# Kernel tuning notes

Hardware: AMD Instinct MI355X
Metric: run time of the kernel (lower is better)

Reference implementation:

```python
import jax, jax.numpy as jnp
import numpy as np

B, R, D, G = 1024, 256, 512, 4
BETA_GROUP = 6.0
BETA_K = 8.0
INIT_KAPPA = 6.0


def setup_inputs() -> dict:
    key = jax.random.key(0)
    ks = jax.random.split(key, 9)
    f32 = jnp.float32
    return {
        "x": jax.random.normal(ks[0], (B, D), f32),
        "th": 0.1 * jax.random.normal(ks[1], (R, D), f32),
        "ineq_sign_param": 0.1 * jax.random.normal(ks[2], (R, D), f32),
        "e_sign_param": 0.1 * jax.random.normal(ks[3], (R, D), f32),
        "mask_logit": jnp.full((R, D), -2.0, f32) + 0.01 * jax.random.normal(ks[4], (R, D), f32),
        "log_kappa": jnp.asarray(np.log(INIT_KAPPA), f32),
        "group_logits": 0.1 * jax.random.normal(ks[5], (G, D), f32),
        "tg": 0.1 * jax.random.normal(ks[6], (R, G), f32),
        "gmask_logit": jnp.full((R, G), -1.0, f32) + 0.01 * jax.random.normal(ks[7], (R, G), f32),
        "k_frac_param": jnp.zeros((R,), f32),
        "head_w": 0.01 * jax.random.normal(ks[8], (1, R), f32),
        "head_b": jnp.zeros((1,), f32),
    }


def reference(x, th, ineq_sign_param, e_sign_param, mask_logit, log_kappa,
              group_logits, tg, gmask_logit, k_frac_param, head_w, head_b):
    kappa = jnp.clip(jnp.exp(log_kappa), 0.5, 50.0)
    ineq = jnp.tanh(ineq_sign_param)                       # (R, D)
    # c: (B, R, D) sharp per-feature comparison
    c = jax.nn.sigmoid(kappa * ineq[None] * (x[:, None, :] - th[None]))
    m = jax.nn.sigmoid(mask_logit)                         # (R, D)
    e_sign = jnp.tanh(e_sign_param)                        # (R, D)
    sym = (m * e_sign)[None] * (2.0 * c - 1.0)             # (B, R, D)
    A = jax.nn.softmax(group_logits, axis=0)               # (G, D)
    eg = jnp.einsum('brd,gd->brg', sym, A)                 # (B, R, G)
    pg = jax.nn.sigmoid(BETA_GROUP * (eg - tg[None]))
    gmask = jax.nn.sigmoid(gmask_logit)                    # (R, G)
    score = jnp.sum(pg * gmask[None], axis=2)              # (B, R)
    enabled = jnp.sum(gmask, axis=1)[None] + 1e-6          # (1, R)
    k = jax.nn.sigmoid(k_frac_param)[None] * enabled       # (1, R)
    z = jax.nn.sigmoid(BETA_K * (score - k))               # (B, R)
    y = z @ head_w.T + head_b                              # (B, 1)
    return y.squeeze(-1)
```

## Files before the change

### kernel.cpp

```cpp
#include <hip/hip_runtime.h>

#define B 1024
#define R 256
#define D 512
#define G 4

#define LOG2E 1.44269504088896340736f

#define OFF_FA   0
#define OFF_FB   (R*D)
#define OFF_SAG  (2*R*D)
#define OFF_EPI  (2*R*D + G*R*D)
#define OFF_PART (OFF_EPI + R*12)
#define NRG 32
#define NBG 16

__device__ __forceinline__ float sig_precise(float v) {
    return 1.0f / (1.0f + expf(-v));
}

__global__ __launch_bounds__(256)
void sge_precompute(const float* __restrict__ th,  const float* __restrict__ isp,
                    const float* __restrict__ esp, const float* __restrict__ ml,
                    const float* __restrict__ lk,  const float* __restrict__ gl,
                    const float* __restrict__ tg,  const float* __restrict__ gml,
                    const float* __restrict__ kf,  const float* __restrict__ hw,
                    float* __restrict__ ws)
{
    const int r   = blockIdx.x;
    const int tid = threadIdx.x;
    __shared__ float4 red[256];

    float kappa = expf(lk[0]);
    kappa = fminf(fmaxf(kappa, 0.5f), 50.0f);

    float4 psum = make_float4(0.f, 0.f, 0.f, 0.f);
    for (int d = tid; d < D; d += 256) {
        const int idx = r * D + d;
        const float thv  = th[idx];
        const float ineq = tanhf(isp[idx]);
        const float es   = tanhf(esp[idx]);
        const float mm   = sig_precise(ml[idx]);
        const float g0 = gl[0*D + d], g1 = gl[1*D + d], g2 = gl[2*D + d], g3 = gl[3*D + d];
        const float mx = fmaxf(fmaxf(g0, g1), fmaxf(g2, g3));
        const float e0 = expf(g0 - mx), e1 = expf(g1 - mx), e2 = expf(g2 - mx), e3 = expf(g3 - mx);
        const float inv = 1.0f / (e0 + e1 + e2 + e3);
        const float a0 = e0 * inv, a1 = e1 * inv, a2 = e2 * inv, a3 = e3 * inv;

        const float fa = -kappa * ineq * LOG2E;
        const float fb = -fa * thv;
        const float s  = mm * es;
        const float s0 = s * a0, s1 = s * a1, s2 = s * a2, s3 = s * a3;

        ws[OFF_FA + idx] = fa;
        ws[OFF_FB + idx] = fb;
        ws[OFF_SAG + (r * G + 0) * D + d] = s0;
        ws[OFF_SAG + (r * G + 1) * D + d] = s1;
        ws[OFF_SAG + (r * G + 2) * D + d] = s2;
        ws[OFF_SAG + (r * G + 3) * D + d] = s3;
        psum.x += s0; psum.y += s1; psum.z += s2; psum.w += s3;
    }
    red[tid] = psum;
    __syncthreads();
    for (int s = 128; s > 0; s >>= 1) {
        if (tid < s) {
            red[tid].x += red[tid + s].x;
            red[tid].y += red[tid + s].y;
            red[tid].z += red[tid + s].z;
            red[tid].w += red[tid + s].w;
        }
        __syncthreads();
    }
    if (tid == 0) {
        const float4 base = red[0];
        const float gm0 = sig_precise(gml[r * G + 0]);
        const float gm1 = sig_precise(gml[r * G + 1]);
        const float gm2 = sig_precise(gml[r * G + 2]);
        const float gm3 = sig_precise(gml[r * G + 3]);
        const float en  = gm0 + gm1 + gm2 + gm3 + 1e-6f;
        const float k   = sig_precise(kf[r]) * en;
        float* epi = ws + OFF_EPI + r * 12;
        epi[0] = 6.0f * (base.x + tg[r * G + 0]) * LOG2E;
        epi[1] = 6.0f * (base.y + tg[r * G + 1]) * LOG2E;
        epi[2] = 6.0f * (base.z + tg[r * G + 2]) * LOG2E;
        epi[3] = 6.0f * (base.w + tg[r * G + 3]) * LOG2E;
        epi[4] = gm0; epi[5] = gm1; epi[6] = gm2; epi[7] = gm3;
        epi[8] = 8.0f * k * LOG2E;
        epi[9] = hw[r];
        epi[10] = 0.f; epi[11] = 0.f;
    }
}

__global__ __launch_bounds__(512, 4)
void sge_main(const float* __restrict__ x, const float* __restrict__ ws,
              float* __restrict__ part)
{
    __shared__ float xl[64 * 260];
    __shared__ float zbuf[512];

    const int tid  = threadIdx.x;
    const int lane = tid & 63;
    const int w    = __builtin_amdgcn_readfirstlane(tid >> 6);
    const int bg   = blockIdx.x;
    const int rg   = blockIdx.y;
    const int r    = rg * 8 + w;

    const float* fa_p = ws + OFF_FA + r * D;
    const float* fb_p = ws + OFF_FB + r * D;
    const float* s0_p = ws + OFF_SAG + (r * G + 0) * D;
    const float* s1_p = s0_p + D;
    const float* s2_p = s1_p + D;
    const float* s3_p = s2_p + D;

    float acc0 = 0.f, acc1 = 0.f, acc2 = 0.f, acc3 = 0.f;

    for (int h = 0; h < 2; ++h) {
        __syncthreads();
        for (int i = tid; i < 64 * 64; i += 512) {
            const int row = i >> 6, c4 = i & 63;
            const float4 v = reinterpret_cast<const float4*>(x)[(bg * 64 + row) * (D / 4) + h * 64 + c4];
            *reinterpret_cast<float4*>(&xl[row * 260 + c4 * 4]) = v;
        }
        __syncthreads();

        const int dbase = h * 256;
        for (int d0 = 0; d0 < 256; d0 += 8) {
            float fa[8], fb[8], q0[8], q1[8], q2[8], q3[8];
            #pragma unroll
            for (int k = 0; k < 8; ++k) {
                fa[k] = fa_p[dbase + d0 + k];
                fb[k] = fb_p[dbase + d0 + k];
                q0[k] = s0_p[dbase + d0 + k];
                q1[k] = s1_p[dbase + d0 + k];
                q2[k] = s2_p[dbase + d0 + k];
                q3[k] = s3_p[dbase + d0 + k];
            }
            const float4 xa = *reinterpret_cast<const float4*>(&xl[lane * 260 + d0]);
            const float4 xb = *reinterpret_cast<const float4*>(&xl[lane * 260 + d0 + 4]);
            const float xs[8] = {xa.x, xa.y, xa.z, xa.w, xb.x, xb.y, xb.z, xb.w};
            #pragma unroll
            for (int k = 0; k < 8; ++k) {
                const float t = fmaf(fa[k], xs[k], fb[k]);
                const float q = __builtin_amdgcn_exp2f(t);
                const float c = __builtin_amdgcn_rcpf(1.0f + q);
                acc0 = fmaf(q0[k], c, acc0);
                acc1 = fmaf(q1[k], c, acc1);
                acc2 = fmaf(q2[k], c, acc2);
                acc3 = fmaf(q3[k], c, acc3);
            }
        }
    }

    const float* epi = ws + OFF_EPI + r * 12;
    const float C12 = -12.0f * LOG2E;
    const float C8  = -8.0f  * LOG2E;
    const float pg0 = __builtin_amdgcn_rcpf(1.0f + __builtin_amdgcn_exp2f(fmaf(C12, acc0, epi[0])));
    const float pg1 = __builtin_amdgcn_rcpf(1.0f + __builtin_amdgcn_exp2f(fmaf(C12, acc1, epi[1])));
    const float pg2 = __builtin_amdgcn_rcpf(1.0f + __builtin_amdgcn_exp2f(fmaf(C12, acc2, epi[2])));
    const float pg3 = __builtin_amdgcn_rcpf(1.0f + __builtin_amdgcn_exp2f(fmaf(C12, acc3, epi[3])));
    float score = pg0 * epi[4];
    score = fmaf(pg1, epi[5], score);
    score = fmaf(pg2, epi[6], score);
    score = fmaf(pg3, epi[7], score);
    const float z = __builtin_amdgcn_rcpf(1.0f + __builtin_amdgcn_exp2f(fmaf(C8, score, epi[8])));
    zbuf[tid] = epi[9] * z;
    __syncthreads();
    if (tid < 64) {
        float s = zbuf[tid];
        #pragma unroll
        for (int ww = 1; ww < 8; ++ww) s += zbuf[ww * 64 + tid];
        part[rg * B + bg * 64 + tid] = s;
    }
}

__global__ __launch_bounds__(256)
void sge_finalize(const float* __restrict__ part, const float* __restrict__ hb,
                  float* __restrict__ y)
{
    const int b = blockIdx.x * 256 + threadIdx.x;
    float s = hb[0];
    #pragma unroll
    for (int rg = 0; rg < NRG; ++rg) s += part[rg * B + b];
    y[b] = s;
}

extern "C" void kernel_launch(void* const* d_in, const int* in_sizes, int n_in,
                              void* d_out, int out_size, void* d_ws, size_t ws_size,
                              hipStream_t stream)
{
    const float* x   = (const float*)d_in[0];
    const float* th  = (const float*)d_in[1];
    const float* isp = (const float*)d_in[2];
    const float* esp = (const float*)d_in[3];
    const float* ml  = (const float*)d_in[4];
    const float* lk  = (const float*)d_in[5];
    const float* gl  = (const float*)d_in[6];
    const float* tg  = (const float*)d_in[7];
    const float* gml = (const float*)d_in[8];
    const float* kf  = (const float*)d_in[9];
    const float* hw  = (const float*)d_in[10];
    const float* hb  = (const float*)d_in[11];
    float* ws = (float*)d_ws;
    float* y  = (float*)d_out;

    sge_precompute<<<R, 256, 0, stream>>>(th, isp, esp, ml, lk, gl, tg, gml, kf, hw, ws);
    sge_main<<<dim3(NBG, NRG), 512, 0, stream>>>(x, ws, ws + OFF_PART);
    sge_finalize<<<B / 256, 256, 0, stream>>>(ws + OFF_PART, hb, y);
}
```

Baseline: 62.74 us.

## Interleave per-chunk params, double-buffer loads, use packed FP32 math and shared reciprocal

Precompute now stores per-rule parameters interleaved in 48-float chunks (theta, fa, four group scales), so each 8-feature step reads one contiguous block instead of six strided arrays. The main loop double-buffers these parameter loads and the x values from shared memory across chunks. The inner math uses 2-wide float vectors for packed FP32 operations and computes one reciprocal per pair of sigmoids. The aim is to cut the transcendental (rcp) count and hide the wave-uniform load latency, at the cost of more registers, slightly different rounding, and a possible overflow in the product of two (1+q) terms when kappa*|x-th| is large.

Measured after the change: 55.83 us. -11.0%, faster.

```diff
diff --git a/kernel.cpp b/kernel.cpp
--- a/kernel.cpp
+++ b/kernel.cpp
@@ -7,13 +7,15 @@
 
 #define LOG2E 1.44269504088896340736f
 
-#define OFF_FA   0
-#define OFF_FB   (R*D)
-#define OFF_SAG  (2*R*D)
-#define OFF_EPI  (2*R*D + G*R*D)
+#define OFF_PB   0
+#define OFF_EPI  (R*64*48)
 #define OFF_PART (OFF_EPI + R*12)
 #define NRG 32
 #define NBG 16
+
+typedef float f2 __attribute__((ext_vector_type(2)));
+
+static __device__ __forceinline__ f2 mk2(float a, float b) { f2 v; v.x = a; v.y = b; return v; }
 
 __device__ __forceinline__ float sig_precise(float v) {
     return 1.0f / (1.0f + expf(-v));
@@ -48,16 +50,17 @@
         const float a0 = e0 * inv, a1 = e1 * inv, a2 = e2 * inv, a3 = e3 * inv;
 
         const float fa = -kappa * ineq * LOG2E;
-        const float fb = -fa * thv;
         const float s  = mm * es;
         const float s0 = s * a0, s1 = s * a1, s2 = s * a2, s3 = s * a3;
 
-        ws[OFF_FA + idx] = fa;
-        ws[OFF_FB + idx] = fb;
-        ws[OFF_SAG + (r * G + 0) * D + d] = s0;
-        ws[OFF_SAG + (r * G + 1) * D + d] = s1;
-        ws[OFF_SAG + (r * G + 2) * D + d] = s2;
-        ws[OFF_SAG + (r * G + 3) * D + d] = s3;
+        const int chunk = d >> 3, j = d & 7;
+        float* pc = ws + OFF_PB + (size_t)(r * 64 + chunk) * 48;
+        pc[j]      = thv;
+        pc[8 + j]  = fa;
+        pc[16 + j] = s0;
+        pc[24 + j] = s1;
+        pc[32 + j] = s2;
+        pc[40 + j] = s3;
         psum.x += s0; psum.y += s1; psum.z += s2; psum.w += s3;
     }
     red[tid] = psum;
@@ -105,14 +108,33 @@
     const int rg   = blockIdx.y;
     const int r    = rg * 8 + w;
 
-    const float* fa_p = ws + OFF_FA + r * D;
-    const float* fb_p = ws + OFF_FB + r * D;
-    const float* s0_p = ws + OFF_SAG + (r * G + 0) * D;
-    const float* s1_p = s0_p + D;
-    const float* s2_p = s1_p + D;
-    const float* s3_p = s2_p + D;
-
-    float acc0 = 0.f, acc1 = 0.f, acc2 = 0.f, acc3 = 0.f;
+    const float* pb = ws + OFF_PB + (size_t)r * (64 * 48);
+
+    f2 acc0 = mk2(0.f, 0.f), acc1 = mk2(0.f, 0.f), acc2 = mk2(0.f, 0.f), acc3 = mk2(0.f, 0.f);
+
+    float pA[48], pB[48];
+    float4 xaA, xbA, xaB, xbB;
+
+    auto compute = [&](const float (&p)[48], const float4& xa, const float4& xb) {
+        const float xs[8] = {xa.x, xa.y, xa.z, xa.w, xb.x, xb.y, xb.z, xb.w};
+        #pragma unroll
+        for (int i = 0; i < 4; ++i) {
+            const f2 xp  = mk2(xs[2*i],        xs[2*i + 1]);
+            const f2 th2 = mk2(p[2*i],         p[2*i + 1]);
+            const f2 fa2 = mk2(p[8  + 2*i],    p[9  + 2*i]);
+            const f2 t   = (xp - th2) * fa2;
+            f2 q;
+            q.x = __builtin_amdgcn_exp2f(t.x);
+            q.y = __builtin_amdgcn_exp2f(t.y);
+            const f2 a = q + 1.0f;
+            const float rp = __builtin_amdgcn_rcpf(a.x * a.y);
+            const f2 c = mk2(a.y * rp, a.x * rp);
+            acc0 = __builtin_elementwise_fma(mk2(p[16 + 2*i], p[17 + 2*i]), c, acc0);
+            acc1 = __builtin_elementwise_fma(mk2(p[24 + 2*i], p[25 + 2*i]), c, acc1);
+            acc2 = __builtin_elementwise_fma(mk2(p[32 + 2*i], p[33 + 2*i]), c, acc2);
+            acc3 = __builtin_elementwise_fma(mk2(p[40 + 2*i], p[41 + 2*i]), c, acc3);
+        }
+    };
 
     for (int h = 0; h < 2; ++h) {
         __syncthreads();
@@ -123,41 +145,47 @@
         }
         __syncthreads();
 
-        const int dbase = h * 256;
-        for (int d0 = 0; d0 < 256; d0 += 8) {
-            float fa[8], fb[8], q0[8], q1[8], q2[8], q3[8];
+        {
+            const float* pc = pb + (h * 32) * 48;
             #pragma unroll
-            for (int k = 0; k < 8; ++k) {
-                fa[k] = fa_p[dbase + d0 + k];
-                fb[k] = fb_p[dbase + d0 + k];
-                q0[k] = s0_p[dbase + d0 + k];
-                q1[k] = s1_p[dbase + d0 + k];
-                q2[k] = s2_p[dbase + d0 + k];
-                q3[k] = s3_p[dbase + d0 + k];
+            for (int j = 0; j < 48; ++j) pA[j] = pc[j];
+            xaA = *reinterpret_cast<const float4*>(&xl[lane * 260 + 0]);
+            xbA = *reinterpret_cast<const float4*>(&xl[lane * 260 + 4]);
+        }
+        #pragma unroll 1
+        for (int c = 0; c < 32; c += 2) {
+            {
+                const float* pc = pb + (h * 32 + c + 1) * 48;
+                #pragma unroll
+                for (int j = 0; j < 48; ++j) pB[j] = pc[j];
+                xaB = *reinterpret_cast<const float4*>(&xl[lane * 260 + (c + 1) * 8]);
+                xbB = *reinterpret_cast<const float4*>(&xl[lane * 260 + (c + 1) * 8 + 4]);
             }
-            const float4 xa = *reinterpret_cast<const float4*>(&xl[lane * 260 + d0]);
-            const float4 xb = *reinterpret_cast<const float4*>(&xl[lane * 260 + d0 + 4]);
-            const float xs[8] = {xa.x, xa.y, xa.z, xa.w, xb.x, xb.y, xb.z, xb.w};
-            #pragma unroll
-            for (int k = 0; k < 8; ++k) {
-                const float t = fmaf(fa[k], xs[k], fb[k]);
-                const float q = __builtin_amdgcn_exp2f(t);
-                const float c = __builtin_amdgcn_rcpf(1.0f + q);
-                acc0 = fmaf(q0[k], c, acc0);
-                acc1 = fmaf(q1[k], c, acc1);
-                acc2 = fmaf(q2[k], c, acc2);
-                acc3 = fmaf(q3[k], c, acc3);
+            compute(pA, xaA, xbA);
+            {
+                const int cn = (c + 2 < 32) ? (c + 2) : 0;
+                const float* pc = pb + (h * 32 + cn) * 48;
+                #pragma unroll
+                for (int j = 0; j < 48; ++j) pA[j] = pc[j];
+                xaA = *reinterpret_cast<const float4*>(&xl[lane * 260 + cn * 8]);
+                xbA = *reinterpret_cast<const float4*>(&xl[lane * 260 + cn * 8 + 4]);
             }
-        }
-    }
+            compute(pB, xaB, xbB);
+        }
+    }
+
+    const float a0 = acc0.x + acc0.y;
+    const float a1 = acc1.x + acc1.y;
+    const float a2 = acc2.x + acc2.y;
+    const float a3 = acc3.x + acc3.y;
 
     const float* epi = ws + OFF_EPI + r * 12;
     const float C12 = -12.0f * LOG2E;
     const float C8  = -8.0f  * LOG2E;
-    const float pg0 = __builtin_amdgcn_rcpf(1.0f + __builtin_amdgcn_exp2f(fmaf(C12, acc0, epi[0])));
-    const float pg1 = __builtin_amdgcn_rcpf(1.0f + __builtin_amdgcn_exp2f(fmaf(C12, acc1, epi[1])));
-    const float pg2 = __builtin_amdgcn_rcpf(1.0f + __builtin_amdgcn_exp2f(fmaf(C12, acc2, epi[2])));
-    const float pg3 = __builtin_amdgcn_rcpf(1.0f + __builtin_amdgcn_exp2f(fmaf(C12, acc3, epi[3])));
+    const float pg0 = __builtin_amdgcn_rcpf(1.0f + __builtin_amdgcn_exp2f(fmaf(C12, a0, epi[0])));
+    const float pg1 = __builtin_amdgcn_rcpf(1.0f + __builtin_amdgcn_exp2f(fmaf(C12, a1, epi[1])));
+    const float pg2 = __builtin_amdgcn_rcpf(1.0f + __builtin_amdgcn_exp2f(fmaf(C12, a2, epi[2])));
+    const float pg3 = __builtin_amdgcn_rcpf(1.0f + __builtin_amdgcn_exp2f(fmaf(C12, a3, epi[3])));
     float score = pg0 * epi[4];
     score = fmaf(pg1, epi[5], score);
     score = fmaf(pg2, epi[6], score);
```

## Interleave per-rule params, split D across blocks, batch reciprocals, move epilogue to finalize

Applied to the files above, without the earlier changes.

Parameters are repacked into interleaved 24-float chunks per (rule, 4 features) so each wave reads one contiguous record. Each wave now handles two rules over half of D, with a software-pipelined double-buffered loop. Four sigmoid reciprocals are replaced by one rcp plus multiplies, using packed float2 math. Partial group sums per D-half go to the workspace, and the nonlinear epilogue moves into a finalize kernel. Precompute also switches to fast exp2/rcp approximations, which slightly lowers accuracy, and the products of four (1+q) terms can overflow to inf for large exponents.

Result: slower. 71.92 us (+14.6%).

```diff
diff --git a/kernel.cpp b/kernel.cpp
--- a/kernel.cpp
+++ b/kernel.cpp
@@ -7,16 +7,20 @@
 
 #define LOG2E 1.44269504088896340736f
 
-#define OFF_FA   0
-#define OFF_FB   (R*D)
-#define OFF_SAG  (2*R*D)
-#define OFF_EPI  (2*R*D + G*R*D)
+#define OFF_PB   0
+#define OFF_EPI  (R*128*24)
 #define OFF_PART (OFF_EPI + R*12)
-#define NRG 32
-#define NBG 16
-
-__device__ __forceinline__ float sig_precise(float v) {
-    return 1.0f / (1.0f + expf(-v));
+#define NBT 16
+
+typedef float f2 __attribute__((ext_vector_type(2)));
+static __device__ __forceinline__ f2 mk2(float a, float b) { f2 v; v.x = a; v.y = b; return v; }
+
+__device__ __forceinline__ float rcp_f(float v)  { return __builtin_amdgcn_rcpf(v); }
+__device__ __forceinline__ float exp2_f(float v) { return __builtin_amdgcn_exp2f(v); }
+__device__ __forceinline__ float sig_f(float v)  { return rcp_f(1.0f + exp2_f(-v * LOG2E)); }
+__device__ __forceinline__ float tanh_f(float v) {
+    const float q2 = exp2_f(v * (2.0f * LOG2E));
+    return (q2 - 1.0f) * rcp_f(q2 + 1.0f);
 }
 
 __global__ __launch_bounds__(256)
@@ -31,33 +35,35 @@
     const int tid = threadIdx.x;
     __shared__ float4 red[256];
 
-    float kappa = expf(lk[0]);
+    float kappa = exp2_f(lk[0] * LOG2E);
     kappa = fminf(fmaxf(kappa, 0.5f), 50.0f);
 
     float4 psum = make_float4(0.f, 0.f, 0.f, 0.f);
     for (int d = tid; d < D; d += 256) {
         const int idx = r * D + d;
         const float thv  = th[idx];
-        const float ineq = tanhf(isp[idx]);
-        const float es   = tanhf(esp[idx]);
-        const float mm   = sig_precise(ml[idx]);
+        const float ineq = tanh_f(isp[idx]);
+        const float es   = tanh_f(esp[idx]);
+        const float mm   = sig_f(ml[idx]);
         const float g0 = gl[0*D + d], g1 = gl[1*D + d], g2 = gl[2*D + d], g3 = gl[3*D + d];
         const float mx = fmaxf(fmaxf(g0, g1), fmaxf(g2, g3));
-        const float e0 = expf(g0 - mx), e1 = expf(g1 - mx), e2 = expf(g2 - mx), e3 = expf(g3 - mx);
+        const float e0 = exp2_f((g0 - mx) * LOG2E), e1 = exp2_f((g1 - mx) * LOG2E);
+        const float e2 = exp2_f((g2 - mx) * LOG2E), e3 = exp2_f((g3 - mx) * LOG2E);
         const float inv = 1.0f / (e0 + e1 + e2 + e3);
         const float a0 = e0 * inv, a1 = e1 * inv, a2 = e2 * inv, a3 = e3 * inv;
 
         const float fa = -kappa * ineq * LOG2E;
-        const float fb = -fa * thv;
         const float s  = mm * es;
         const float s0 = s * a0, s1 = s * a1, s2 = s * a2, s3 = s * a3;
 
-        ws[OFF_FA + idx] = fa;
-        ws[OFF_FB + idx] = fb;
-        ws[OFF_SAG + (r * G + 0) * D + d] = s0;
-        ws[OFF_SAG + (r * G + 1) * D + d] = s1;
-        ws[OFF_SAG + (r * G + 2) * D + d] = s2;
-        ws[OFF_SAG + (r * G + 3) * D + d] = s3;
+        const int chunk = d >> 2, j = d & 3;
+        float* pc = ws + OFF_PB + ((size_t)r * 128 + chunk) * 24;
+        pc[j]      = thv;
+        pc[4 + j]  = fa;
+        pc[8 + j]  = s0;
+        pc[12 + j] = s1;
+        pc[16 + j] = s2;
+        pc[20 + j] = s3;
         psum.x += s0; psum.y += s1; psum.z += s2; psum.w += s3;
     }
     red[tid] = psum;
@@ -73,12 +79,12 @@
     }
     if (tid == 0) {
         const float4 base = red[0];
-        const float gm0 = sig_precise(gml[r * G + 0]);
-        const float gm1 = sig_precise(gml[r * G + 1]);
-        const float gm2 = sig_precise(gml[r * G + 2]);
-        const float gm3 = sig_precise(gml[r * G + 3]);
+        const float gm0 = sig_f(gml[r * G + 0]);
+        const float gm1 = sig_f(gml[r * G + 1]);
+        const float gm2 = sig_f(gml[r * G + 2]);
+        const float gm3 = sig_f(gml[r * G + 3]);
         const float en  = gm0 + gm1 + gm2 + gm3 + 1e-6f;
-        const float k   = sig_precise(kf[r]) * en;
+        const float k   = sig_f(kf[r]) * en;
         float* epi = ws + OFF_EPI + r * 12;
         epi[0] = 6.0f * (base.x + tg[r * G + 0]) * LOG2E;
         epi[1] = 6.0f * (base.y + tg[r * G + 1]) * LOG2E;
@@ -96,92 +102,135 @@
               float* __restrict__ part)
 {
     __shared__ float xl[64 * 260];
-    __shared__ float zbuf[512];
 
     const int tid  = threadIdx.x;
     const int lane = tid & 63;
     const int w    = __builtin_amdgcn_readfirstlane(tid >> 6);
-    const int bg   = blockIdx.x;
-    const int rg   = blockIdx.y;
-    const int r    = rg * 8 + w;
-
-    const float* fa_p = ws + OFF_FA + r * D;
-    const float* fb_p = ws + OFF_FB + r * D;
-    const float* s0_p = ws + OFF_SAG + (r * G + 0) * D;
-    const float* s1_p = s0_p + D;
-    const float* s2_p = s1_p + D;
-    const float* s3_p = s2_p + D;
-
-    float acc0 = 0.f, acc1 = 0.f, acc2 = 0.f, acc3 = 0.f;
-
-    for (int h = 0; h < 2; ++h) {
-        __syncthreads();
-        for (int i = tid; i < 64 * 64; i += 512) {
-            const int row = i >> 6, c4 = i & 63;
-            const float4 v = reinterpret_cast<const float4*>(x)[(bg * 64 + row) * (D / 4) + h * 64 + c4];
-            *reinterpret_cast<float4*>(&xl[row * 260 + c4 * 4]) = v;
-        }
-        __syncthreads();
-
-        const int dbase = h * 256;
-        for (int d0 = 0; d0 < 256; d0 += 8) {
-            float fa[8], fb[8], q0[8], q1[8], q2[8], q3[8];
-            #pragma unroll
-            for (int k = 0; k < 8; ++k) {
-                fa[k] = fa_p[dbase + d0 + k];
-                fb[k] = fb_p[dbase + d0 + k];
-                q0[k] = s0_p[dbase + d0 + k];
-                q1[k] = s1_p[dbase + d0 + k];
-                q2[k] = s2_p[dbase + d0 + k];
-                q3[k] = s3_p[dbase + d0 + k];
-            }
-            const float4 xa = *reinterpret_cast<const float4*>(&xl[lane * 260 + d0]);
-            const float4 xb = *reinterpret_cast<const float4*>(&xl[lane * 260 + d0 + 4]);
-            const float xs[8] = {xa.x, xa.y, xa.z, xa.w, xb.x, xb.y, xb.z, xb.w};
-            #pragma unroll
-            for (int k = 0; k < 8; ++k) {
-                const float t = fmaf(fa[k], xs[k], fb[k]);
-                const float q = __builtin_amdgcn_exp2f(t);
-                const float c = __builtin_amdgcn_rcpf(1.0f + q);
-                acc0 = fmaf(q0[k], c, acc0);
-                acc1 = fmaf(q1[k], c, acc1);
-                acc2 = fmaf(q2[k], c, acc2);
-                acc3 = fmaf(q3[k], c, acc3);
-            }
-        }
-    }
-
-    const float* epi = ws + OFF_EPI + r * 12;
+    const int bt   = blockIdx.x;
+    const int rbdh = blockIdx.y;
+    const int rblk = rbdh >> 1;
+    const int dh   = rbdh & 1;
+    const int r0   = rblk * 16 + 2 * w;
+    const int r1   = r0 + 1;
+
+    const float* pb0 = ws + OFF_PB + (size_t)r0 * (128 * 24) + (size_t)dh * (64 * 24);
+    const float* pb1 = ws + OFF_PB + (size_t)r1 * (128 * 24) + (size_t)dh * (64 * 24);
+
+    for (int i = tid; i < 64 * 64; i += 512) {
+        const int row = i >> 6, c4 = i & 63;
+        const float4 v = *reinterpret_cast<const float4*>(
+            &x[(size_t)(bt * 64 + row) * D + dh * 256 + c4 * 4]);
+        *reinterpret_cast<float4*>(&xl[row * 260 + c4 * 4]) = v;
+    }
+    __syncthreads();
+
+    f2 a00 = mk2(0.f,0.f), a01 = mk2(0.f,0.f), a02 = mk2(0.f,0.f), a03 = mk2(0.f,0.f);
+    f2 a10 = mk2(0.f,0.f), a11 = mk2(0.f,0.f), a12 = mk2(0.f,0.f), a13 = mk2(0.f,0.f);
+
+    float p0A[24], p0B[24], p1A[24], p1B[24];
+    float4 xA, xB;
+
+    auto loadP = [](float (&p)[24], const float* base, int c) {
+        const float* pc = base + (size_t)c * 24;
+        #pragma unroll
+        for (int j = 0; j < 24; ++j) p[j] = pc[j];
+    };
+    auto loadX = [&](float4& xq, int c) {
+        xq = *reinterpret_cast<const float4*>(&xl[lane * 260 + c * 4]);
+    };
+    auto compute = [](const float (&p)[24], const float4& xq,
+                      f2& g0, f2& g1, f2& g2, f2& g3) {
+        const f2 x0 = mk2(xq.x, xq.y), x1 = mk2(xq.z, xq.w);
+        const f2 t0 = (x0 - mk2(p[0], p[1])) * mk2(p[4], p[5]);
+        const f2 t1 = (x1 - mk2(p[2], p[3])) * mk2(p[6], p[7]);
+        f2 q0, q1;
+        q0.x = exp2_f(t0.x); q0.y = exp2_f(t0.y);
+        q1.x = exp2_f(t1.x); q1.y = exp2_f(t1.y);
+        const f2 b0 = q0 + 1.0f, b1 = q1 + 1.0f;
+        const float P0 = b0.x * b0.y, P1 = b1.x * b1.y;
+        const float r4 = rcp_f(P0 * P1);
+        const float i0 = r4 * P1, i1 = r4 * P0;
+        const f2 c0 = __builtin_shufflevector(b0, b0, 1, 0) * i0;
+        const f2 c1 = __builtin_shufflevector(b1, b1, 1, 0) * i1;
+        g0 = __builtin_elementwise_fma(mk2(p[8],  p[9]),  c0, g0);
+        g0 = __builtin_elementwise_fma(mk2(p[10], p[11]), c1, g0);
+        g1 = __builtin_elementwise_fma(mk2(p[12], p[13]), c0, g1);
+        g1 = __builtin_elementwise_fma(mk2(p[14], p[15]), c1, g1);
+        g2 = __builtin_elementwise_fma(mk2(p[16], p[17]), c0, g2);
+        g2 = __builtin_elementwise_fma(mk2(p[18], p[19]), c1, g2);
+        g3 = __builtin_elementwise_fma(mk2(p[20], p[21]), c0, g3);
+        g3 = __builtin_elementwise_fma(mk2(p[22], p[23]), c1, g3);
+    };
+
+    loadP(p0A, pb0, 0); loadP(p1A, pb1, 0); loadX(xA, 0);
+
+    #pragma unroll 1
+    for (int c = 0; c < 64; c += 2) {
+        loadX(xB, c + 1);
+        loadP(p0B, pb0, c + 1);
+        compute(p0A, xA, a00, a01, a02, a03);
+        loadP(p1B, pb1, c + 1);
+        compute(p1A, xA, a10, a11, a12, a13);
+        const int cn = (c + 2 < 64) ? (c + 2) : 0;
+        loadX(xA, cn);
+        loadP(p0A, pb0, cn);
+        compute(p0B, xB, a00, a01, a02, a03);
+        loadP(p1A, pb1, cn);
+        compute(p1B, xB, a10, a11, a12, a13);
+    }
+
+    {
+        float4 v0 = make_float4(a00.x + a00.y, a01.x + a01.y, a02.x + a02.y, a03.x + a03.y);
+        float4 v1 = make_float4(a10.x + a10.y, a11.x + a11.y, a12.x + a12.y, a13.x + a13.y);
+        float* pa0 = part + ((size_t)(r0 * 2 + dh) * B + bt * 64 + lane) * 4;
+        float* pa1 = part + ((size_t)(r1 * 2 + dh) * B + bt * 64 + lane) * 4;
+        *reinterpret_cast<float4*>(pa0) = v0;
+        *reinterpret_cast<float4*>(pa1) = v1;
+    }
+}
+
+__global__ __launch_bounds__(512)
+void sge_finalize(const float* __restrict__ part, const float* __restrict__ ws,
+                  const float* __restrict__ hb, float* __restrict__ y)
+{
+    __shared__ float red[512];
+    const int tid   = threadIdx.x;
+    const int lane  = tid & 63;
+    const int slice = tid >> 6;
+    const int bg    = blockIdx.x;
+    const int b     = bg * 64 + lane;
     const float C12 = -12.0f * LOG2E;
     const float C8  = -8.0f  * LOG2E;
-    const float pg0 = __builtin_amdgcn_rcpf(1.0f + __builtin_amdgcn_exp2f(fmaf(C12, acc0, epi[0])));
-    const float pg1 = __builtin_amdgcn_rcpf(1.0f + __builtin_amdgcn_exp2f(fmaf(C12, acc1, epi[1])));
-    const float pg2 = __builtin_amdgcn_rcpf(1.0f + __builtin_amdgcn_exp2f(fmaf(C12, acc2, epi[2])));
-    const float pg3 = __builtin_amdgcn_rcpf(1.0f + __builtin_amdgcn_exp2f(fmaf(C12, acc3, epi[3])));
-    float score = pg0 * epi[4];
-    score = fmaf(pg1, epi[5], score);
-    score = fmaf(pg2, epi[6], score);
-    score = fmaf(pg3, epi[7], score);
-    const float z = __builtin_amdgcn_rcpf(1.0f + __builtin_amdgcn_exp2f(fmaf(C8, score, epi[8])));
-    zbuf[tid] = epi[9] * z;
+
+    float s = 0.f;
+    for (int rr = 0; rr < 32; ++rr) {
+        const int r = slice * 32 + rr;
+        const float4 v0 = *reinterpret_cast<const float4*>(part + ((size_t)(r * 2 + 0) * B + b) * 4);
+        const float4 v1 = *reinterpret_cast<const float4*>(part + ((size_t)(r * 2 + 1) * B + b) * 4);
+        const float a0 = v0.x + v1.x;
+        const float a1 = v0.y + v1.y;
+        const float a2 = v0.z + v1.z;
+        const float a3 = v0.w + v1.w;
+        const float* epi = ws + OFF_EPI + r * 12;
+        const float pg0 = rcp_f(1.0f + exp2_f(fmaf(C12, a0, epi[0])));
+        const float pg1 = rcp_f(1.0f + exp2_f(fmaf(C12, a1, epi[1])));
+        const float pg2 = rcp_f(1.0f + exp2_f(fmaf(C12, a2, epi[2])));
+        const float pg3 = rcp_f(1.0f + exp2_f(fmaf(C12, a3, epi[3])));
+        float score = pg0 * epi[4];
+        score = fmaf(pg1, epi[5], score);
+        score = fmaf(pg2, epi[6], score);
+        score = fmaf(pg3, epi[7], score);
+        const float z = rcp_f(1.0f + exp2_f(fmaf(C8, score, epi[8])));
+        s = fmaf(epi[9], z, s);
+    }
+    red[tid] = s;
     __syncthreads();
-    if (tid < 64) {
-        float s = zbuf[tid];
+    if (slice == 0) {
+        float tot = hb[0];
         #pragma unroll
-        for (int ww = 1; ww < 8; ++ww) s += zbuf[ww * 64 + tid];
-        part[rg * B + bg * 64 + tid] = s;
-    }
-}
-
-__global__ __launch_bounds__(256)
-void sge_finalize(const float* __restrict__ part, const float* __restrict__ hb,
-                  float* __restrict__ y)
-{
-    const int b = blockIdx.x * 256 + threadIdx.x;
-    float s = hb[0];
-    #pragma unroll
-    for (int rg = 0; rg < NRG; ++rg) s += part[rg * B + b];
-    y[b] = s;
+        for (int k = 0; k < 8; ++k) tot += red[k * 64 + lane];
+        y[b] = tot;
+    }
 }
 
 extern "C" void kernel_launch(void* const* d_in, const int* in_sizes, int n_in,
@@ -204,6 +253,6 @@
     float* y  = (float*)d_out;
 
     sge_precompute<<<R, 256, 0, stream>>>(th, isp, esp, ml, lk, gl, tg, gml, kf, hw, ws);
-    sge_main<<<dim3(NBG, NRG), 512, 0, stream>>>(x, ws, ws + OFF_PART);
-    sge_finalize<<<B / 256, 256, 0, stream>>>(ws + OFF_PART, hb, y);
-}
+    sge_main<<<dim3(NBT, 32), 512, 0, stream>>>(x, ws, ws + OFF_PART);
+    sge_finalize<<<NBT, 512, 0, stream>>>(ws + OFF_PART, ws, hb, y);
+}
```
